# Kernel optimization log

Measured on AMD Instinct MI355X. Metric: run time of the kernel, lower is better.

Reference implementation:

```python
import jax, jax.numpy as jnp
import numpy as np

D_MODEL = 512
D_ALPHA = 100
D_PH = 80
SCALE = 1.0 / np.sqrt(D_MODEL)


def gru_cell(x, h, Wih, Whh, bih, bhh):
    # PyTorch GRU gate order: r, z, n
    gi = x @ Wih.T + bih
    gh = h @ Whh.T + bhh
    ir, iz, inn = jnp.split(gi, 3, axis=-1)
    hr, hz, hn = jnp.split(gh, 3, axis=-1)
    r = jax.nn.sigmoid(ir + hr)
    z = jax.nn.sigmoid(iz + hz)
    n = jnp.tanh(inn + r * hn)
    return (1.0 - z) * n + z * h


def attend(q, k, v):
    # q: [B,D], k/v: [B,L,D]
    scores = jnp.einsum('bd,bld->bl', q, k) * SCALE
    a = jax.nn.softmax(scores, axis=-1)  # [B,L]
    o = jnp.einsum('bl,bld->bd', a, v)
    return a, o


def setup_inputs() -> dict:
    key = jax.random.key(0)
    ks = jax.random.split(key, 25)
    D = D_MODEL

    def u(k, shape, fan):
        return jax.random.uniform(k, shape, jnp.float32, -1.0, 1.0) / np.sqrt(fan)

    inp = {
        'text': jax.random.randint(ks[0], (256, 128), 0, D_ALPHA),
        'tgt': jax.random.randint(ks[1], (256, 64), 0, D_PH),
        'E_alpha': jax.random.normal(ks[2], (D_ALPHA, D), jnp.float32),
        'enc_Wih_f': u(ks[3], (3 * D, D), D),
        'enc_Whh_f': u(ks[4], (3 * D, D), D),
        'enc_bih_f': u(ks[5], (3 * D,), D),
        'enc_bhh_f': u(ks[6], (3 * D,), D),
        'enc_Wih_b': u(ks[7], (3 * D, D), D),
        'enc_Whh_b': u(ks[8], (3 * D, D), D),
        'enc_bih_b': u(ks[9], (3 * D,), D),
        'enc_bhh_b': u(ks[10], (3 * D,), D),
        'hpost_W': u(ks[11], (D, 2 * D), 2 * D),
        'hpost_b': u(ks[12], (D,), 2 * D),
        'wk_W': u(ks[13], (D, 2 * D), 2 * D),
        'wk_b': u(ks[14], (D,), 2 * D),
        'wv_W': u(ks[15], (D, 2 * D), 2 * D),
        'wv_b': u(ks[16], (D,), 2 * D),
        'E_ph': jax.random.normal(ks[17], (D_PH, D), jnp.float32),
        'dec_Wih': u(ks[18], (3 * D, 2 * D), 2 * D),
        'dec_Whh': u(ks[19], (3 * D, D), D),
        'dec_bih': u(ks[20], (3 * D,), D),
        'dec_bhh': u(ks[21], (3 * D,), D),
        'post_W': u(ks[22], (D_PH, D), D),
        'post_b': u(ks[23], (D_PH,), D),
    }
    return inp


def reference(text, tgt, E_alpha, enc_Wih_f, enc_Whh_f, enc_bih_f, enc_bhh_f,
              enc_Wih_b, enc_Whh_b, enc_bih_b, enc_bhh_b, hpost_W, hpost_b,
              wk_W, wk_b, wv_W, wv_b, E_ph, dec_Wih, dec_Whh, dec_bih,
              dec_bhh, post_W, post_b):
    B, LT = text.shape
    LP = tgt.shape[1]

    # ---- Encoder: bidirectional single-layer GRU (eval: dropout = identity)
    emb = E_alpha[text]                     # [B,LT,D]
    xs = jnp.swapaxes(emb, 0, 1)            # [LT,B,D]
    h0 = jnp.zeros((B, D_MODEL), emb.dtype)

    def mk_step(Wih, Whh, bih, bhh):
        def step(h, x):
            h2 = gru_cell(x, h, Wih, Whh, bih, bhh)
            return h2, h2
        return step

    hF, ysF = jax.lax.scan(mk_step(enc_Wih_f, enc_Whh_f, enc_bih_f, enc_bhh_f), h0, xs)
    hB, ysB = jax.lax.scan(mk_step(enc_Wih_b, enc_Whh_b, enc_bih_b, enc_bhh_b), h0, xs[::-1])
    ysB = ysB[::-1]
    enc_o = jnp.swapaxes(jnp.concatenate([ysF, ysB], axis=-1), 0, 1)  # [B,LT,2D]
    h = jnp.tanh(jnp.concatenate([hF, hB], axis=-1) @ hpost_W.T + hpost_b)  # [B,D]

    k = enc_o @ wk_W.T + wk_b               # [B,LT,D]
    v = enc_o @ wv_W.T + wv_b               # [B,LT,D]

    # ---- initial attention from encoder hidden; eval-mode first token is argmax
    # over tgt[:,0] reshaped to [B,1,1], i.e. always index 0.
    a_sl0, a_o0 = attend(h, k, v)
    dec_i0 = jnp.zeros((B,), jnp.int32)

    def dstep(carry, _):
        hh, a_o, a_sl, dec_i = carry
        e = E_ph[dec_i]                                  # [B,D]
        x = gru_cell(jnp.concatenate([e, a_o], axis=-1), hh,
                     dec_Wih, dec_Whh, dec_bih, dec_bhh)  # [B,D]
        o = x @ post_W.T + post_b                         # [B,D_PH]
        n_sl, n_o = attend(x, k, v)
        nxt = jnp.argmax(o, axis=-1).astype(jnp.int32)
        return (x, n_o, n_sl, nxt), (a_sl, o)

    _, (attn_t, res_t) = jax.lax.scan(dstep, (h, a_o0, a_sl0, dec_i0), None, length=LP)
    attn = jnp.swapaxes(attn_t, 0, 1)        # [B,LP,LT]
    res = jnp.swapaxes(res_t, 0, 1)          # [B,LP,D_PH]
    return attn, res
```

## Files before the change

### kernel.cpp

```cpp
#include <hip/hip_runtime.h>
#include <math.h>

#define B   256
#define LT  128
#define LP  64
#define DM  512
#define D3  1536
#define DPH 80
#define SCALE_F 0.044194173824159216f

__device__ __forceinline__ float dot4(float4 a, float4 b) {
    return a.x*b.x + a.y*b.y + a.z*b.z + a.w*b.w;
}
__device__ __forceinline__ float sigmoidf_(float x) {
    return 1.0f / (1.0f + expf(-x));
}

__global__ __launch_bounds__(256) void precompG_kernel(
    const float* __restrict__ Emb, const float* __restrict__ W,
    const float* __restrict__ bias, float* __restrict__ G,
    int wstride, int woff)
{
    const int n  = blockIdx.x * 256 + threadIdx.x;
    const int r0 = blockIdx.y * 4;
    __shared__ float es[4][DM];
    for (int i = threadIdx.x; i < 4 * DM; i += 256)
        es[i >> 9][i & 511] = Emb[(r0 + (i >> 9)) * DM + (i & 511)];
    __syncthreads();
    float acc[4] = {0.f, 0.f, 0.f, 0.f};
    const float* wr = &W[(size_t)n * wstride + woff];
    for (int j = 0; j < DM; j += 4) {
        float4 w4 = *(const float4*)&wr[j];
        #pragma unroll
        for (int rr = 0; rr < 4; ++rr) {
            float4 e4 = *(const float4*)&es[rr][j];
            acc[rr] += dot4(e4, w4);
        }
    }
    float bv = bias[n];
    #pragma unroll
    for (int rr = 0; rr < 4; ++rr)
        G[(r0 + rr) * D3 + n] = acc[rr] + bv;
}

__global__ __launch_bounds__(256) void enc_step_kernel(
    const float* __restrict__ Gf, const float* __restrict__ Gb,
    const float* __restrict__ Whh_f, const float* __restrict__ Whh_b,
    const float* __restrict__ bhh_f, const float* __restrict__ bhh_b,
    const int* __restrict__ text,
    const float* __restrict__ hF_in, float* __restrict__ hF_out,
    const float* __restrict__ hB_in, float* __restrict__ hB_out,
    float* __restrict__ E,
    int s)
{
    const int dir = blockIdx.z;
    const int t   = (dir == 0) ? s : (LT - 1 - s);
    const int yoff = (dir == 0) ? 0 : DM;
    const float* G   = (dir == 0) ? Gf    : Gb;
    const float* Whh = (dir == 0) ? Whh_f : Whh_b;
    const float* bhh = (dir == 0) ? bhh_f : bhh_b;
    const float* hin = (dir == 0) ? hF_in : hB_in;
    float* hout      = (dir == 0) ? hF_out : hB_out;

    __shared__ float As[2][32][36];
    __shared__ float Bs[2][96][36];

    const int tid = threadIdx.x;
    const int jj  = tid & 15;
    const int bb  = tid >> 4;
    const int jtile = blockIdx.x * 32;
    const int btile = blockIdx.y * 32;

    float acc[2][2][3];
    #pragma unroll
    for (int m = 0; m < 2; ++m)
        #pragma unroll
        for (int js = 0; js < 2; ++js)
            #pragma unroll
            for (int g = 0; g < 3; ++g) acc[m][js][g] = 0.f;

    const int lrow = tid >> 3;
    const int lcol = (tid & 7) * 4;
    const int g_  = lrow >> 5;

    int wrow[3];
    #pragma unroll
    for (int rr = 0; rr < 3; ++rr) {
        int brow = lrow + rr * 32;
        wrow[rr] = (brow >> 5) * DM + jtile + (brow & 31);
    }
    (void)g_;

    float4 rA = *(const float4*)&hin[(btile + lrow) * DM + lcol];
    float4 rB0 = *(const float4*)&Whh[(size_t)wrow[0] * DM + lcol];
    float4 rB1 = *(const float4*)&Whh[(size_t)wrow[1] * DM + lcol];
    float4 rB2 = *(const float4*)&Whh[(size_t)wrow[2] * DM + lcol];

    int buf = 0;
    for (int k = 0; k < 16; ++k) {
        *(float4*)&As[buf][lrow][lcol]      = rA;
        *(float4*)&Bs[buf][lrow][lcol]      = rB0;
        *(float4*)&Bs[buf][lrow + 32][lcol] = rB1;
        *(float4*)&Bs[buf][lrow + 64][lcol] = rB2;
        __syncthreads();
        if (k < 15) {
            const int k0 = (k + 1) * 32;
            rA  = *(const float4*)&hin[(btile + lrow) * DM + k0 + lcol];
            rB0 = *(const float4*)&Whh[(size_t)wrow[0] * DM + k0 + lcol];
            rB1 = *(const float4*)&Whh[(size_t)wrow[1] * DM + k0 + lcol];
            rB2 = *(const float4*)&Whh[(size_t)wrow[2] * DM + k0 + lcol];
        }
        #pragma unroll
        for (int c4 = 0; c4 < 8; ++c4) {
            float4 av[2], bv[2][3];
            #pragma unroll
            for (int m = 0; m < 2; ++m)
                av[m] = *(float4*)&As[buf][bb * 2 + m][c4 * 4];
            #pragma unroll
            for (int js = 0; js < 2; ++js)
                #pragma unroll
                for (int g = 0; g < 3; ++g)
                    bv[js][g] = *(float4*)&Bs[buf][g * 32 + jj + 16 * js][c4 * 4];
            #pragma unroll
            for (int m = 0; m < 2; ++m)
                #pragma unroll
                for (int js = 0; js < 2; ++js)
                    #pragma unroll
                    for (int g = 0; g < 3; ++g)
                        acc[m][js][g] += dot4(av[m], bv[js][g]);
        }
        buf ^= 1;
    }

    #pragma unroll
    for (int m = 0; m < 2; ++m) {
        const int b = btile + bb * 2 + m;
        const int c = text[b * LT + t];
        #pragma unroll
        for (int js = 0; js < 2; ++js) {
            const int j = jtile + jj + 16 * js;
            float hr = acc[m][js][0] + bhh[j];
            float hz = acc[m][js][1] + bhh[DM + j];
            float hn = acc[m][js][2] + bhh[2 * DM + j];
            float r = sigmoidf_(G[c * D3 + j] + hr);
            float z = sigmoidf_(G[c * D3 + DM + j] + hz);
            float n = tanhf(G[c * D3 + 2 * DM + j] + r * hn);
            float hp = hin[b * DM + j];
            float hv = (1.f - z) * n + z * hp;
            hout[b * DM + j] = hv;
            E[(size_t)(b * LT + t) * 1024 + yoff + j] = hv;
        }
    }
}

__global__ __launch_bounds__(256) void kv_chunk_kernel(
    const float* __restrict__ E,
    const float* __restrict__ wk, const float* __restrict__ wv,
    const float* __restrict__ kb, const float* __restrict__ vb,
    float* __restrict__ T, int r0)
{
    __shared__ float As[64][36];
    __shared__ float Bk[64][36];
    __shared__ float Bv[64][36];
    const int tid = threadIdx.x;
    const int nn = tid & 15, bb = tid >> 4;
    const int ntile = blockIdx.x * 64;
    const int mtile = blockIdx.y * 64;

    float ak[4][4], av_[4][4];
    #pragma unroll
    for (int m = 0; m < 4; ++m)
        #pragma unroll
        for (int i = 0; i < 4; ++i) { ak[m][i] = 0.f; av_[m][i] = 0.f; }

    const int lrow = tid >> 3;
    const int lcol = (tid & 7) * 4;

    for (int k0 = 0; k0 < 1024; k0 += 32) {
        __syncthreads();
        *(float4*)&As[lrow][lcol] =
            *(const float4*)&E[(size_t)(r0 + mtile + lrow) * 1024 + k0 + lcol];
        *(float4*)&As[lrow + 32][lcol] =
            *(const float4*)&E[(size_t)(r0 + mtile + lrow + 32) * 1024 + k0 + lcol];
        *(float4*)&Bk[lrow][lcol] =
            *(const float4*)&wk[(ntile + lrow) * 1024 + k0 + lcol];
        *(float4*)&Bk[lrow + 32][lcol] =
            *(const float4*)&wk[(ntile + lrow + 32) * 1024 + k0 + lcol];
        *(float4*)&Bv[lrow][lcol] =
            *(const float4*)&wv[(ntile + lrow) * 1024 + k0 + lcol];
        *(float4*)&Bv[lrow + 32][lcol] =
            *(const float4*)&wv[(ntile + lrow + 32) * 1024 + k0 + lcol];
        __syncthreads();
        #pragma unroll
        for (int c4 = 0; c4 < 8; ++c4) {
            float4 a4[4], k4[4], v4[4];
            #pragma unroll
            for (int m = 0; m < 4; ++m) a4[m] = *(float4*)&As[bb + 16 * m][c4 * 4];
            #pragma unroll
            for (int i = 0; i < 4; ++i) {
                k4[i] = *(float4*)&Bk[nn + 16 * i][c4 * 4];
                v4[i] = *(float4*)&Bv[nn + 16 * i][c4 * 4];
            }
            #pragma unroll
            for (int m = 0; m < 4; ++m)
                #pragma unroll
                for (int i = 0; i < 4; ++i) {
                    ak[m][i]  += dot4(a4[m], k4[i]);
                    av_[m][i] += dot4(a4[m], v4[i]);
                }
        }
    }
    #pragma unroll
    for (int m = 0; m < 4; ++m) {
        const int lm = mtile + bb + 16 * m;
        #pragma unroll
        for (int i = 0; i < 4; ++i) {
            const int gn = ntile + nn + 16 * i;
            T[(size_t)lm * 1024 + gn]       = ak[m][i]  + kb[gn];
            T[(size_t)lm * 1024 + DM + gn]  = av_[m][i] + vb[gn];
        }
    }
}

__global__ __launch_bounds__(256) void hpost_kernel(
    const float* __restrict__ hF, const float* __restrict__ hB,
    const float* __restrict__ W, const float* __restrict__ bias,
    float* __restrict__ out)
{
    const int b = blockIdx.x;
    __shared__ float as_[1024];
    for (int i = threadIdx.x; i < DM; i += 256) {
        as_[i]      = hF[b * DM + i];
        as_[DM + i] = hB[b * DM + i];
    }
    __syncthreads();
    for (int n = threadIdx.x; n < DM; n += 256) {
        const float* wr = &W[n * 1024];
        float acc = 0.f;
        for (int j = 0; j < 1024; j += 4)
            acc += dot4(*(const float4*)&as_[j], *(const float4*)&wr[j]);
        out[b * DM + n] = tanhf(acc + bias[n]);
    }
}

__global__ __launch_bounds__(256) void dec_step_kernel(
    const float* __restrict__ Gd,
    const float* __restrict__ dec_Wih, const float* __restrict__ dec_Whh,
    const float* __restrict__ bhh,
    const int* __restrict__ dec_i,
    const float* __restrict__ a_o,
    const float* __restrict__ h_in, float* __restrict__ h_out)
{
    __shared__ float As[2][16][36];
    __shared__ float Bs[2][96][36];
    const int tid = threadIdx.x;
    const int jj = tid & 15, bb = tid >> 4;
    const int jtile = blockIdx.x * 32;
    const int btile = blockIdx.y * 16;

    float acc[2][4];
    #pragma unroll
    for (int js = 0; js < 2; ++js)
        #pragma unroll
        for (int g = 0; g < 4; ++g) acc[js][g] = 0.f;

    const int lrow  = tid >> 3;
    const int lcol  = (tid & 7) * 4;
    const int lrowA = lrow;

    int wrow[3];
    #pragma unroll
    for (int rr = 0; rr < 3; ++rr) {
        int brow = lrow + rr * 32;
        wrow[rr] = (brow >> 5) * DM + jtile + (brow & 31);
    }

    float4 rA = make_float4(0.f,0.f,0.f,0.f), rB0, rB1, rB2;
    {
        if (tid < 128)
            rA = *(const float4*)&a_o[(btile + lrowA) * DM + lcol];
        rB0 = *(const float4*)&dec_Wih[(size_t)wrow[0] * 1024 + DM + lcol];
        rB1 = *(const float4*)&dec_Wih[(size_t)wrow[1] * 1024 + DM + lcol];
        rB2 = *(const float4*)&dec_Wih[(size_t)wrow[2] * 1024 + DM + lcol];
    }

    int buf = 0;
    for (int kk = 0; kk < 32; ++kk) {
        const int phase = kk >> 4;
        if (tid < 128)
            *(float4*)&As[buf][lrowA][lcol] = rA;
        *(float4*)&Bs[buf][lrow][lcol]      = rB0;
        *(float4*)&Bs[buf][lrow + 32][lcol] = rB1;
        *(float4*)&Bs[buf][lrow + 64][lcol] = rB2;
        __syncthreads();
        if (kk < 31) {
            const int nk = kk + 1;
            const int np = nk >> 4;
            const int k0 = (nk & 15) * 32;
            if (tid < 128) {
                const float* Aptr = (np == 0) ? a_o : h_in;
                rA = *(const float4*)&Aptr[(btile + lrowA) * DM + k0 + lcol];
            }
            if (np == 0) {
                rB0 = *(const float4*)&dec_Wih[(size_t)wrow[0] * 1024 + DM + k0 + lcol];
                rB1 = *(const float4*)&dec_Wih[(size_t)wrow[1] * 1024 + DM + k0 + lcol];
                rB2 = *(const float4*)&dec_Wih[(size_t)wrow[2] * 1024 + DM + k0 + lcol];
            } else {
                rB0 = *(const float4*)&dec_Whh[(size_t)wrow[0] * DM + k0 + lcol];
                rB1 = *(const float4*)&dec_Whh[(size_t)wrow[1] * DM + k0 + lcol];
                rB2 = *(const float4*)&dec_Whh[(size_t)wrow[2] * DM + k0 + lcol];
            }
        }
        #pragma unroll
        for (int c4 = 0; c4 < 8; ++c4) {
            float4 av = *(float4*)&As[buf][bb][c4 * 4];
            float4 bv[2][3];
            #pragma unroll
            for (int js = 0; js < 2; ++js)
                #pragma unroll
                for (int g = 0; g < 3; ++g)
                    bv[js][g] = *(float4*)&Bs[buf][g * 32 + jj + 16 * js][c4 * 4];
            #pragma unroll
            for (int js = 0; js < 2; ++js) {
                acc[js][0]         += dot4(av, bv[js][0]);
                acc[js][1]         += dot4(av, bv[js][1]);
                acc[js][2 + phase] += dot4(av, bv[js][2]);
            }
        }
        buf ^= 1;
    }

    const int b = btile + bb;
    const int c = dec_i[b];
    #pragma unroll
    for (int js = 0; js < 2; ++js) {
        const int j = jtile + jj + 16 * js;
        float r = sigmoidf_(Gd[c * D3 + j] + bhh[j] + acc[js][0]);
        float z = sigmoidf_(Gd[c * D3 + DM + j] + bhh[DM + j] + acc[js][1]);
        float n = tanhf(Gd[c * D3 + 2 * DM + j] + acc[js][2]
                        + r * (acc[js][3] + bhh[2 * DM + j]));
        float hp = h_in[b * DM + j];
        h_out[b * DM + j] = (1.f - z) * n + z * hp;
    }
}

__global__ __launch_bounds__(256) void dec_attend_post_kernel(
    const float* __restrict__ q,
    const float* __restrict__ EKV,
    const float* __restrict__ post_W, const float* __restrict__ post_b,
    float* __restrict__ attn, float* __restrict__ res,
    float* __restrict__ a_o, int* __restrict__ dec_i,
    int s, int attn_row, int do_post, int do_attn)
{
    const int b = blockIdx.x;
    const int tid = threadIdx.x;
    __shared__ float qs[DM];
    __shared__ float part[256];
    __shared__ float sarr[LT];
    __shared__ float red[2];
    __shared__ float4 pvp[2][128];

    if (tid < 128)
        *(float4*)&qs[tid * 4] = *(const float4*)&q[b * DM + tid * 4];
    __syncthreads();

    if (do_post) {
        if (tid < DPH) {
            const float* wr = &post_W[tid * DM];
            float acc = 0.f;
            for (int d = 0; d < DM; d += 4)
                acc += dot4(*(const float4*)&qs[d], *(const float4*)&wr[d]);
            float lv = acc + post_b[tid];
            res[(b * LP + s) * DPH + tid] = lv;
            part[tid] = lv;
        }
        __syncthreads();
        if (tid == 0) {
            float best = part[0]; int bi = 0;
            for (int p = 1; p < DPH; ++p) {
                float vv = part[p];
                if (vv > best) { best = vv; bi = p; }
            }
            dec_i[b] = bi;
        }
        __syncthreads();
    }

    if (do_attn) {
        {
            const int r = tid & 127, half = tid >> 7;
            const float* kr = &EKV[(size_t)(b * LT + r) * 1024 + half * 256];
            const float* qh = &qs[half * 256];
            float p = 0.f;
            #pragma unroll
            for (int d = 0; d < 256; d += 4)
                p += dot4(*(const float4*)&qh[d], *(const float4*)&kr[d]);
            part[tid] = p;
        }
        __syncthreads();
        if (tid < LT) sarr[tid] = (part[tid] + part[tid + 128]) * SCALE_F;
        __syncthreads();
        if (tid < 64) {
            float m = fmaxf(sarr[tid], sarr[tid + 64]);
            #pragma unroll
            for (int off = 32; off > 0; off >>= 1)
                m = fmaxf(m, __shfl_xor(m, off));
            if (tid == 0) red[0] = m;
        }
        __syncthreads();
        const float smax = red[0];
        if (tid < LT) sarr[tid] = expf(sarr[tid] - smax);
        __syncthreads();
        if (tid < 64) {
            float ssum = sarr[tid] + sarr[tid + 64];
            #pragma unroll
            for (int off = 32; off > 0; off >>= 1)
                ssum += __shfl_xor(ssum, off);
            if (tid == 0) red[1] = ssum;
        }
        __syncthreads();
        const float inv = 1.0f / red[1];
        if (tid < LT) {
            float a = sarr[tid] * inv;
            sarr[tid] = a;
            attn[(size_t)(b * LP + attn_row) * LT + tid] = a;
        }
        __syncthreads();
        {
            const int d4 = tid & 127, half = tid >> 7;
            const float* vb0 = &EKV[(size_t)b * LT * 1024 + DM];
            float4 acc = make_float4(0.f, 0.f, 0.f, 0.f);
            const int l0 = half * 64;
            #pragma unroll 8
            for (int l = l0; l < l0 + 64; ++l) {
                float a = sarr[l];
                float4 v4 = *(const float4*)&vb0[(size_t)l * 1024 + d4 * 4];
                acc.x += a * v4.x; acc.y += a * v4.y;
                acc.z += a * v4.z; acc.w += a * v4.w;
            }
            pvp[half][d4] = acc;
        }
        __syncthreads();
        if (tid < 128) {
            float4 p0 = pvp[0][tid], p1 = pvp[1][tid];
            float4 o = make_float4(p0.x + p1.x, p0.y + p1.y,
                                   p0.z + p1.z, p0.w + p1.w);
            *(float4*)&a_o[b * DM + tid * 4] = o;
        }
    }
}

extern "C" void kernel_launch(void* const* d_in, const int* in_sizes, int n_in,
                              void* d_out, int out_size, void* d_ws, size_t ws_size,
                              hipStream_t stream)
{
    const int*   text    = (const int*)d_in[0];
    const float* E_alpha = (const float*)d_in[2];
    const float* Wih_f   = (const float*)d_in[3];
    const float* Whh_f   = (const float*)d_in[4];
    const float* bih_f   = (const float*)d_in[5];
    const float* bhh_f   = (const float*)d_in[6];
    const float* Wih_b   = (const float*)d_in[7];
    const float* Whh_b   = (const float*)d_in[8];
    const float* bih_b   = (const float*)d_in[9];
    const float* bhh_b   = (const float*)d_in[10];
    const float* hpost_W = (const float*)d_in[11];
    const float* hpost_b = (const float*)d_in[12];
    const float* wk_W    = (const float*)d_in[13];
    const float* wk_b    = (const float*)d_in[14];
    const float* wv_W    = (const float*)d_in[15];
    const float* wv_b    = (const float*)d_in[16];
    const float* E_ph    = (const float*)d_in[17];
    const float* dec_Wih = (const float*)d_in[18];
    const float* dec_Whh = (const float*)d_in[19];
    const float* dec_bih = (const float*)d_in[20];
    const float* dec_bhh = (const float*)d_in[21];
    const float* post_W  = (const float*)d_in[22];
    const float* post_b  = (const float*)d_in[23];

    float* ws = (float*)d_ws;
    float* Gf  = ws;
    float* Gb  = Gf  + 153600;
    float* Gd  = Gb  + 153600;
    float* hF0 = Gd  + 122880;
    float* hF1 = hF0 + 131072;
    float* hB0 = hF1 + 131072;
    float* hB1 = hB0 + 131072;
    float* hd0 = hB1 + 131072;
    float* hd1 = hd0 + 131072;
    float* a_o = hd1 + 131072;
    int*   dec_i = (int*)(a_o + 131072);
    float* E   = a_o + 131072 + 512;
    float* T   = E + 33554432;

    hipMemsetAsync(hF0, 0, 131072 * sizeof(float), stream);
    hipMemsetAsync(hB0, 0, 131072 * sizeof(float), stream);
    hipMemsetAsync(dec_i, 0, B * sizeof(int), stream);

    precompG_kernel<<<dim3(6, 25), 256, 0, stream>>>(E_alpha, Wih_f, bih_f, Gf, DM, 0);
    precompG_kernel<<<dim3(6, 25), 256, 0, stream>>>(E_alpha, Wih_b, bih_b, Gb, DM, 0);
    precompG_kernel<<<dim3(6, 20), 256, 0, stream>>>(E_ph, dec_Wih, dec_bih, Gd, 1024, 0);

    for (int s = 0; s < LT; ++s) {
        const float* fin = (s & 1) ? hF1 : hF0;
        float*       fou = (s & 1) ? hF0 : hF1;
        const float* bin = (s & 1) ? hB1 : hB0;
        float*       bou = (s & 1) ? hB0 : hB1;
        enc_step_kernel<<<dim3(16, 8, 2), 256, 0, stream>>>(
            Gf, Gb, Whh_f, Whh_b, bhh_f, bhh_b, text,
            fin, fou, bin, bou, E, s);
    }

    for (int c = 0; c < 4; ++c) {
        const int r0 = c * 8192;
        kv_chunk_kernel<<<dim3(8, 128), 256, 0, stream>>>(
            E, wk_W, wv_W, wk_b, wv_b, T, r0);
        hipMemcpyAsync(E + (size_t)r0 * 1024, T,
                       (size_t)8192 * 1024 * sizeof(float),
                       hipMemcpyDeviceToDevice, stream);
    }

    hpost_kernel<<<dim3(B), 256, 0, stream>>>(hF0, hB0, hpost_W, hpost_b, hd0);

    float* attn = (float*)d_out;
    float* res  = attn + (size_t)B * LP * LT;

    dec_attend_post_kernel<<<dim3(B), 256, 0, stream>>>(
        hd0, E, post_W, post_b, attn, res, a_o, dec_i,
        0, 0, 0, 1);

    for (int s = 0; s < LP; ++s) {
        const float* hin = (s & 1) ? hd1 : hd0;
        float*       hou = (s & 1) ? hd0 : hd1;
        dec_step_kernel<<<dim3(16, 16), 256, 0, stream>>>(
            Gd, dec_Wih, dec_Whh, dec_bhh, dec_i, a_o, hin, hou);
        dec_attend_post_kernel<<<dim3(B), 256, 0, stream>>>(
            hou, E, post_W, post_b, attn, res, a_o, dec_i,
            s, s + 1, 1, (s < LP - 1) ? 1 : 0);
    }
}
```

Measured before the change: 11.22 ms.

## Shrink batch tiles in recurrent step kernels to launch more blocks per step

```diff
diff --git a/kernel.cpp b/kernel.cpp
--- a/kernel.cpp
+++ b/kernel.cpp
@@ -62,26 +62,23 @@
     const float* hin = (dir == 0) ? hF_in : hB_in;
     float* hout      = (dir == 0) ? hF_out : hB_out;
 
-    __shared__ float As[2][32][36];
+    __shared__ float As[2][16][36];
     __shared__ float Bs[2][96][36];
 
     const int tid = threadIdx.x;
     const int jj  = tid & 15;
     const int bb  = tid >> 4;
     const int jtile = blockIdx.x * 32;
-    const int btile = blockIdx.y * 32;
-
-    float acc[2][2][3];
-    #pragma unroll
-    for (int m = 0; m < 2; ++m)
-        #pragma unroll
-        for (int js = 0; js < 2; ++js)
-            #pragma unroll
-            for (int g = 0; g < 3; ++g) acc[m][js][g] = 0.f;
+    const int btile = blockIdx.y * 16;
+
+    float acc[2][3];
+    #pragma unroll
+    for (int js = 0; js < 2; ++js)
+        #pragma unroll
+        for (int g = 0; g < 3; ++g) acc[js][g] = 0.f;
 
     const int lrow = tid >> 3;
     const int lcol = (tid & 7) * 4;
-    const int g_  = lrow >> 5;
 
     int wrow[3];
     #pragma unroll
@@ -89,67 +86,63 @@
         int brow = lrow + rr * 32;
         wrow[rr] = (brow >> 5) * DM + jtile + (brow & 31);
     }
-    (void)g_;
-
-    float4 rA = *(const float4*)&hin[(btile + lrow) * DM + lcol];
+
+    float4 rA = make_float4(0.f,0.f,0.f,0.f);
+    if (tid < 128)
+        rA = *(const float4*)&hin[(btile + lrow) * DM + lcol];
     float4 rB0 = *(const float4*)&Whh[(size_t)wrow[0] * DM + lcol];
     float4 rB1 = *(const float4*)&Whh[(size_t)wrow[1] * DM + lcol];
     float4 rB2 = *(const float4*)&Whh[(size_t)wrow[2] * DM + lcol];
 
     int buf = 0;
     for (int k = 0; k < 16; ++k) {
-        *(float4*)&As[buf][lrow][lcol]      = rA;
+        if (tid < 128)
+            *(float4*)&As[buf][lrow][lcol] = rA;
         *(float4*)&Bs[buf][lrow][lcol]      = rB0;
         *(float4*)&Bs[buf][lrow + 32][lcol] = rB1;
         *(float4*)&Bs[buf][lrow + 64][lcol] = rB2;
         __syncthreads();
         if (k < 15) {
             const int k0 = (k + 1) * 32;
-            rA  = *(const float4*)&hin[(btile + lrow) * DM + k0 + lcol];
+            if (tid < 128)
+                rA = *(const float4*)&hin[(btile + lrow) * DM + k0 + lcol];
             rB0 = *(const float4*)&Whh[(size_t)wrow[0] * DM + k0 + lcol];
             rB1 = *(const float4*)&Whh[(size_t)wrow[1] * DM + k0 + lcol];
             rB2 = *(const float4*)&Whh[(size_t)wrow[2] * DM + k0 + lcol];
         }
         #pragma unroll
         for (int c4 = 0; c4 < 8; ++c4) {
-            float4 av[2], bv[2][3];
-            #pragma unroll
-            for (int m = 0; m < 2; ++m)
-                av[m] = *(float4*)&As[buf][bb * 2 + m][c4 * 4];
+            float4 av = *(float4*)&As[buf][bb][c4 * 4];
+            float4 bv[2][3];
             #pragma unroll
             for (int js = 0; js < 2; ++js)
                 #pragma unroll
                 for (int g = 0; g < 3; ++g)
                     bv[js][g] = *(float4*)&Bs[buf][g * 32 + jj + 16 * js][c4 * 4];
             #pragma unroll
-            for (int m = 0; m < 2; ++m)
+            for (int js = 0; js < 2; ++js)
                 #pragma unroll
-                for (int js = 0; js < 2; ++js)
-                    #pragma unroll
-                    for (int g = 0; g < 3; ++g)
-                        acc[m][js][g] += dot4(av[m], bv[js][g]);
+                for (int g = 0; g < 3; ++g)
+                    acc[js][g] += dot4(av, bv[js][g]);
         }
         buf ^= 1;
     }
 
-    #pragma unroll
-    for (int m = 0; m < 2; ++m) {
-        const int b = btile + bb * 2 + m;
-        const int c = text[b * LT + t];
-        #pragma unroll
-        for (int js = 0; js < 2; ++js) {
-            const int j = jtile + jj + 16 * js;
-            float hr = acc[m][js][0] + bhh[j];
-            float hz = acc[m][js][1] + bhh[DM + j];
-            float hn = acc[m][js][2] + bhh[2 * DM + j];
-            float r = sigmoidf_(G[c * D3 + j] + hr);
-            float z = sigmoidf_(G[c * D3 + DM + j] + hz);
-            float n = tanhf(G[c * D3 + 2 * DM + j] + r * hn);
-            float hp = hin[b * DM + j];
-            float hv = (1.f - z) * n + z * hp;
-            hout[b * DM + j] = hv;
-            E[(size_t)(b * LT + t) * 1024 + yoff + j] = hv;
-        }
+    const int b = btile + bb;
+    const int c = text[b * LT + t];
+    #pragma unroll
+    for (int js = 0; js < 2; ++js) {
+        const int j = jtile + jj + 16 * js;
+        float hr = acc[js][0] + bhh[j];
+        float hz = acc[js][1] + bhh[DM + j];
+        float hn = acc[js][2] + bhh[2 * DM + j];
+        float r = sigmoidf_(G[c * D3 + j] + hr);
+        float z = sigmoidf_(G[c * D3 + DM + j] + hz);
+        float n = tanhf(G[c * D3 + 2 * DM + j] + r * hn);
+        float hp = hin[b * DM + j];
+        float hv = (1.f - z) * n + z * hp;
+        hout[b * DM + j] = hv;
+        E[(size_t)(b * LT + t) * 1024 + yoff + j] = hv;
     }
 }
 
@@ -222,6 +215,14 @@
     }
 }
 
+__global__ __launch_bounds__(256) void copy4_kernel(
+    float4* __restrict__ dst, const float4* __restrict__ src, int n4)
+{
+    int i = blockIdx.x * 256 + threadIdx.x;
+    const int stride = gridDim.x * 256;
+    for (; i < n4; i += stride) dst[i] = src[i];
+}
+
 __global__ __launch_bounds__(256) void hpost_kernel(
     const float* __restrict__ hF, const float* __restrict__ hB,
     const float* __restrict__ W, const float* __restrict__ bias,
@@ -251,22 +252,21 @@
     const float* __restrict__ a_o,
     const float* __restrict__ h_in, float* __restrict__ h_out)
 {
-    __shared__ float As[2][16][36];
+    __shared__ float As[2][8][36];
     __shared__ float Bs[2][96][36];
     const int tid = threadIdx.x;
-    const int jj = tid & 15, bb = tid >> 4;
+    const int jj = tid & 15;
+    const int js = (tid >> 4) & 1;
+    const int bb = tid >> 5;
     const int jtile = blockIdx.x * 32;
-    const int btile = blockIdx.y * 16;
-
-    float acc[2][4];
-    #pragma unroll
-    for (int js = 0; js < 2; ++js)
-        #pragma unroll
-        for (int g = 0; g < 4; ++g) acc[js][g] = 0.f;
-
-    const int lrow  = tid >> 3;
-    const int lcol  = (tid & 7) * 4;
-    const int lrowA = lrow;
+    const int btile = blockIdx.y * 8;
+
+    float acc[4];
+    #pragma unroll
+    for (int g = 0; g < 4; ++g) acc[g] = 0.f;
+
+    const int lrow = tid >> 3;
+    const int lcol = (tid & 7) * 4;
 
     int wrow[3];
     #pragma unroll
@@ -276,19 +276,17 @@
     }
 
     float4 rA = make_float4(0.f,0.f,0.f,0.f), rB0, rB1, rB2;
-    {
-        if (tid < 128)
-            rA = *(const float4*)&a_o[(btile + lrowA) * DM + lcol];
-        rB0 = *(const float4*)&dec_Wih[(size_t)wrow[0] * 1024 + DM + lcol];
-        rB1 = *(const float4*)&dec_Wih[(size_t)wrow[1] * 1024 + DM + lcol];
-        rB2 = *(const float4*)&dec_Wih[(size_t)wrow[2] * 1024 + DM + lcol];
-    }
+    if (tid < 64)
+        rA = *(const float4*)&a_o[(btile + lrow) * DM + lcol];
+    rB0 = *(const float4*)&dec_Wih[(size_t)wrow[0] * 1024 + DM + lcol];
+    rB1 = *(const float4*)&dec_Wih[(size_t)wrow[1] * 1024 + DM + lcol];
+    rB2 = *(const float4*)&dec_Wih[(size_t)wrow[2] * 1024 + DM + lcol];
 
     int buf = 0;
     for (int kk = 0; kk < 32; ++kk) {
         const int phase = kk >> 4;
-        if (tid < 128)
-            *(float4*)&As[buf][lrowA][lcol] = rA;
+        if (tid < 64)
+            *(float4*)&As[buf][lrow][lcol] = rA;
         *(float4*)&Bs[buf][lrow][lcol]      = rB0;
         *(float4*)&Bs[buf][lrow + 32][lcol] = rB1;
         *(float4*)&Bs[buf][lrow + 64][lcol] = rB2;
@@ -297,9 +295,9 @@
             const int nk = kk + 1;
             const int np = nk >> 4;
             const int k0 = (nk & 15) * 32;
-            if (tid < 128) {
+            if (tid < 64) {
                 const float* Aptr = (np == 0) ? a_o : h_in;
-                rA = *(const float4*)&Aptr[(btile + lrowA) * DM + k0 + lcol];
+                rA = *(const float4*)&Aptr[(btile + lrow) * DM + k0 + lcol];
             }
             if (np == 0) {
                 rB0 = *(const float4*)&dec_Wih[(size_t)wrow[0] * 1024 + DM + k0 + lcol];
@@ -314,34 +312,26 @@
         #pragma unroll
         for (int c4 = 0; c4 < 8; ++c4) {
             float4 av = *(float4*)&As[buf][bb][c4 * 4];
-            float4 bv[2][3];
-            #pragma unroll
-            for (int js = 0; js < 2; ++js)
-                #pragma unroll
-                for (int g = 0; g < 3; ++g)
-                    bv[js][g] = *(float4*)&Bs[buf][g * 32 + jj + 16 * js][c4 * 4];
-            #pragma unroll
-            for (int js = 0; js < 2; ++js) {
-                acc[js][0]         += dot4(av, bv[js][0]);
-                acc[js][1]         += dot4(av, bv[js][1]);
-                acc[js][2 + phase] += dot4(av, bv[js][2]);
-            }
+            float4 bv[3];
+            #pragma unroll
+            for (int g = 0; g < 3; ++g)
+                bv[g] = *(float4*)&Bs[buf][g * 32 + jj + 16 * js][c4 * 4];
+            acc[0]         += dot4(av, bv[0]);
+            acc[1]         += dot4(av, bv[1]);
+            acc[2 + phase] += dot4(av, bv[2]);
         }
         buf ^= 1;
     }
 
     const int b = btile + bb;
     const int c = dec_i[b];
-    #pragma unroll
-    for (int js = 0; js < 2; ++js) {
-        const int j = jtile + jj + 16 * js;
-        float r = sigmoidf_(Gd[c * D3 + j] + bhh[j] + acc[js][0]);
-        float z = sigmoidf_(Gd[c * D3 + DM + j] + bhh[DM + j] + acc[js][1]);
-        float n = tanhf(Gd[c * D3 + 2 * DM + j] + acc[js][2]
-                        + r * (acc[js][3] + bhh[2 * DM + j]));
-        float hp = h_in[b * DM + j];
-        h_out[b * DM + j] = (1.f - z) * n + z * hp;
-    }
+    const int j = jtile + jj + 16 * js;
+    float r = sigmoidf_(Gd[c * D3 + j] + bhh[j] + acc[0]);
+    float z = sigmoidf_(Gd[c * D3 + DM + j] + bhh[DM + j] + acc[1]);
+    float n = tanhf(Gd[c * D3 + 2 * DM + j] + acc[2]
+                    + r * (acc[3] + bhh[2 * DM + j]));
+    float hp = h_in[b * DM + j];
+    h_out[b * DM + j] = (1.f - z) * n + z * hp;
 }
 
 __global__ __launch_bounds__(256) void dec_attend_post_kernel(
@@ -506,18 +496,18 @@
         float*       fou = (s & 1) ? hF0 : hF1;
         const float* bin = (s & 1) ? hB1 : hB0;
         float*       bou = (s & 1) ? hB0 : hB1;
-        enc_step_kernel<<<dim3(16, 8, 2), 256, 0, stream>>>(
+        enc_step_kernel<<<dim3(16, 16, 2), 256, 0, stream>>>(
             Gf, Gb, Whh_f, Whh_b, bhh_f, bhh_b, text,
             fin, fou, bin, bou, E, s);
     }
 
-    for (int c = 0; c < 4; ++c) {
-        const int r0 = c * 8192;
-        kv_chunk_kernel<<<dim3(8, 128), 256, 0, stream>>>(
+    for (int c = 0; c < 2; ++c) {
+        const int r0 = c * 16384;
+        kv_chunk_kernel<<<dim3(8, 256), 256, 0, stream>>>(
             E, wk_W, wv_W, wk_b, wv_b, T, r0);
-        hipMemcpyAsync(E + (size_t)r0 * 1024, T,
-                       (size_t)8192 * 1024 * sizeof(float),
-                       hipMemcpyDeviceToDevice, stream);
+        copy4_kernel<<<dim3(4096), 256, 0, stream>>>(
+            (float4*)(E + (size_t)r0 * 1024), (const float4*)T,
+            16384 * 1024 / 4);
     }
 
     hpost_kernel<<<dim3(B), 256, 0, stream>>>(hF0, hB0, hpost_W, hpost_b, hd0);
@@ -532,7 +522,7 @@
     for (int s = 0; s < LP; ++s) {
         const float* hin = (s & 1) ? hd1 : hd0;
         float*       hou = (s & 1) ? hd0 : hd1;
-        dec_step_kernel<<<dim3(16, 16), 256, 0, stream>>>(
+        dec_step_kernel<<<dim3(16, 32), 256, 0, stream>>>(
             Gd, dec_Wih, dec_Whh, dec_bhh, dec_i, a_o, hin, hou);
         dec_attend_post_kernel<<<dim3(B), 256, 0, stream>>>(
             hou, E, post_W, post_b, attn, res, a_o, dec_i,
```

Result: faster. 10.54 ms (-6.0%).
